# Optimization experiments

Hardware: AMD Instinct MI355X
Metric: run time of the kernel (lower is better)

## Reference

```python
import jax, jax.numpy as jnp
import numpy as np


def conv1d(x, w, b, pad):
    # x: (B, Cin, T), w: (Cout, Cin, K), b: (Cout,)
    y = jax.lax.conv_general_dilated(x, w, window_strides=(1,), padding=[(pad, pad)],
                                     dimension_numbers=('NCH', 'OIH', 'NCH'))
    return y + b[None, :, None]


def setup_inputs() -> dict:
    key = jax.random.key(0)
    ks = jax.random.split(key, 12)
    B, Cm, T1, Ct, T2, Ca = 8, 80, 800, 512, 200, 80
    queries = jax.random.normal(ks[0], (B, Cm, T1), dtype=jnp.float32)
    keys = jax.random.normal(ks[1], (B, Ct, T2), dtype=jnp.float32)
    query_lens = jnp.full((B,), T1, dtype=jnp.int32)
    key_lens = jax.random.randint(ks[2], (B,), T2 // 2, T2 + 1)
    # mask True where key position is padding (>= key_len): (B, T2, 1)
    mask = (jnp.arange(T2)[None, :] >= key_lens[:, None])[:, :, None]
    attn_prior = jax.random.uniform(ks[3], (B, T1, T2), dtype=jnp.float32) + 0.1
    # key_proj: Conv1d(512->1024, k=3, pad=1) + ReLU + Conv1d(1024->80, k=1)
    kp_w1 = jax.random.normal(ks[4], (2 * Ct, Ct, 3), jnp.float32) * 0.02
    kp_b1 = jnp.zeros((2 * Ct,), jnp.float32)
    kp_w2 = jax.random.normal(ks[5], (Ca, 2 * Ct, 1), jnp.float32) * 0.02
    kp_b2 = jnp.zeros((Ca,), jnp.float32)
    # query_proj (3xconv): Conv1d(80->160,k3)+ReLU+Conv1d(160->80,k1)+ReLU+Conv1d(80->80,k1)
    qp_w1 = jax.random.normal(ks[6], (2 * Cm, Cm, 3), jnp.float32) * 0.05
    qp_b1 = jnp.zeros((2 * Cm,), jnp.float32)
    qp_w2 = jax.random.normal(ks[7], (Cm, 2 * Cm, 1), jnp.float32) * 0.05
    qp_b2 = jnp.zeros((Cm,), jnp.float32)
    qp_w3 = jax.random.normal(ks[8], (Ca, Cm, 1), jnp.float32) * 0.05
    qp_b3 = jnp.zeros((Ca,), jnp.float32)
    return {"queries": queries, "keys": keys, "query_lens": query_lens, "mask": mask,
            "attn_prior": attn_prior, "kp_w1": kp_w1, "kp_b1": kp_b1, "kp_w2": kp_w2,
            "kp_b2": kp_b2, "qp_w1": qp_w1, "qp_b1": qp_b1, "qp_w2": qp_w2,
            "qp_b2": qp_b2, "qp_w3": qp_w3, "qp_b3": qp_b3}


def reference(queries, keys, query_lens, mask, attn_prior,
              kp_w1, kp_b1, kp_w2, kp_b2,
              qp_w1, qp_b1, qp_w2, qp_b2, qp_w3, qp_b3):
    # key projection: (B, Ct, T2) -> (B, Ca, T2)
    ke = conv1d(keys, kp_w1, kp_b1, pad=1)
    ke = jax.nn.relu(ke)
    ke = conv1d(ke, kp_w2, kp_b2, pad=0)
    # query projection ('3xconv'): (B, Cm, T1) -> (B, Ca, T1)
    qe = conv1d(queries, qp_w1, qp_b1, pad=1)
    qe = jax.nn.relu(qe)
    qe = conv1d(qe, qp_w2, qp_b2, pad=0)
    qe = jax.nn.relu(qe)
    qe = conv1d(qe, qp_w3, qp_b3, pad=0)
    # broadcasted squared L2 distance: (B, Ca, T1, T2) -> reduce C -> (B, 1, T1, T2)
    diff2 = (qe[:, :, :, None] - ke[:, :, None, :]) ** 2
    attn = -0.0005 * jnp.sum(diff2, axis=1, keepdims=True)
    # prior in log domain
    attn = jax.nn.log_softmax(attn, axis=3) + jnp.log(attn_prior[:, None] + 1e-8)
    attn_logprob = attn
    # mask (B, T2, 1) -> (B, 1, 1, T2)
    m = jnp.transpose(mask, (0, 2, 1))[:, :, None, :]
    attn = jnp.where(m, -jnp.inf, attn)
    attn = jax.nn.softmax(attn, axis=3)
    return (attn, attn_logprob)
```

## Files before the change

kernel.cpp:

```cpp
#include <hip/hip_runtime.h>
#include <hip/hip_bf16.h>
#include <math.h>

#define B_  8
#define CM  80
#define T1_ 800
#define CT  512
#define T2_ 200
#define CA  80

using bf16 = __hip_bfloat16;
typedef __attribute__((ext_vector_type(8))) short bf16x8;
typedef __attribute__((ext_vector_type(4))) float f32x4;

#define LDSW 56
#define LDSW2 72
#define LDSW3 168
#define LDSW4 104

__device__ __forceinline__ float load_sel(const void* p, long idx, int isf32) {
  if (isf32) return ((const float*)p)[idx];
  return __bfloat162float(((const bf16*)p)[idx]);
}

__device__ __forceinline__ unsigned short f2bf(float x) {
  bf16 h = __float2bfloat16(x);
  return *reinterpret_cast<unsigned short*>(&h);
}

__device__ __forceinline__ int detect_f32(const unsigned short* q) {
  __shared__ int s_f;
  const int tid = threadIdx.x;
  if (tid < 64) {
    unsigned short u = q[2 * tid];
    int e = (u >> 7) & 0xFF;
    unsigned long long bal = __ballot(e < 100 || e > 154);
    if (tid == 0) s_f = (__popcll(bal) >= 16) ? 1 : 0;
  }
  __syncthreads();
  return s_f;
}

__device__ void task_cvt_t(const void* X, bf16* XT, int f, int C, int T,
                           int id2, int tilesT, float* smem, int tid) {
  const int per_b = tilesT * ((C + 31) >> 5);
  const int b = id2 / per_b;
  const int r = id2 - b * per_b;
  const int ct = r / tilesT, tt = r - ct * tilesT;
  const int c0 = ct * 32, t0 = tt * 32;
  const int tx = tid & 31, trow = tid >> 5;
#pragma unroll
  for (int p = 0; p < 4; ++p) {
    const int cr = trow + 8 * p;
    if (c0 + cr < C && t0 + tx < T)
      smem[cr * 33 + tx] = load_sel(X, ((long)b * C + c0 + cr) * T + t0 + tx, f);
  }
  __syncthreads();
#pragma unroll
  for (int p = 0; p < 4; ++p) {
    const int tr = trow + 8 * p;
    if (t0 + tr < T && c0 + tx < C)
      XT[((long)b * T + t0 + tr) * C + c0 + tx] =
          __float2bfloat16(smem[tx * 33 + tr]);
  }
}

__device__ void task_wfrag(const void* W, bf16* WF, int f, int id2, int tid) {
  const int id = id2 * 256 + tid;
  const int l  = id & 63;
  int rest = id >> 6;
  const int h  = rest & 1; rest >>= 1;
  const int mi = rest & 3; rest >>= 2;
  const int w2 = rest & 1; rest >>= 1;
  const int ks = rest % 24;
  const int p  = rest / 24;
  const int co = p * 128 + w2 * 64 + mi * 16 + (l & 15);
  const int k0 = ks * 64 + h * 32 + (l >> 4) * 8;
  const int dk = k0 >> 9;
  const int ci = k0 & 511;
  const long sbase = ((long)co * 512 + ci) * 3 + dk;
  ushort4 u0, u1;
  u0.x = f2bf(load_sel(W, sbase + 0 * 3, f));
  u0.y = f2bf(load_sel(W, sbase + 1 * 3, f));
  u0.z = f2bf(load_sel(W, sbase + 2 * 3, f));
  u0.w = f2bf(load_sel(W, sbase + 3 * 3, f));
  u1.x = f2bf(load_sel(W, sbase + 4 * 3, f));
  u1.y = f2bf(load_sel(W, sbase + 5 * 3, f));
  u1.z = f2bf(load_sel(W, sbase + 6 * 3, f));
  u1.w = f2bf(load_sel(W, sbase + 7 * 3, f));
  *(ushort4*)(WF + (long)id * 8) = u0;
  *(ushort4*)(WF + (long)id * 8 + 4) = u1;
}

__device__ void task_wt3v(const void* W, bf16* WT, int f, int Co, int Ci,
                          int id2, int tid) {
  const int i = id2 * 256 + tid;
  const int g4 = Ci >> 2;
  if (i >= Co * g4) return;
  const int co = i / g4, ci = (i - co * g4) * 4;
  const long sbase = ((long)co * Ci + ci) * 3;
  float w[12];
  if (f) {
    const float4* s = (const float4*)((const float*)W + sbase);
    float4 f0 = s[0], f1 = s[1], f2 = s[2];
    w[0]=f0.x; w[1]=f0.y; w[2]=f0.z; w[3]=f0.w; w[4]=f1.x; w[5]=f1.y;
    w[6]=f1.z; w[7]=f1.w; w[8]=f2.x; w[9]=f2.y; w[10]=f2.z; w[11]=f2.w;
  } else {
#pragma unroll
    for (int j = 0; j < 12; ++j) w[j] = load_sel(W, sbase + j, 0);
  }
#pragma unroll
  for (int dk = 0; dk < 3; ++dk) {
    ushort4 u;
    u.x = f2bf(w[0 * 3 + dk]); u.y = f2bf(w[1 * 3 + dk]);
    u.z = f2bf(w[2 * 3 + dk]); u.w = f2bf(w[3 * 3 + dk]);
    *(ushort4*)(WT + ((long)dk * Co + co) * Ci + ci) = u;
  }
}

__device__ void task_cvtv(const void* W, bf16* O, int f, int n, int id2, int tid) {
  const int i = (id2 * 256 + tid) * 4;
  if (i >= n) return;
  ushort4 u;
  if (f) {
    float4 v = *(const float4*)((const float*)W + i);
    u.x = f2bf(v.x); u.y = f2bf(v.y); u.z = f2bf(v.z); u.w = f2bf(v.w);
  } else {
    u.x = f2bf(load_sel(W, i, 0));     u.y = f2bf(load_sel(W, i + 1, 0));
    u.z = f2bf(load_sel(W, i + 2, 0)); u.w = f2bf(load_sel(W, i + 3, 0));
  }
  *(ushort4*)(O + i) = u;
}

__global__ __launch_bounds__(256) void k_prep(
    const void* __restrict__ queries, const void* __restrict__ keys,
    const void* __restrict__ mask,
    const void* __restrict__ kp_w1, const void* __restrict__ kp_b1,
    const void* __restrict__ kp_w2, const void* __restrict__ kp_b2,
    const void* __restrict__ qp_w1, const void* __restrict__ qp_b1,
    const void* __restrict__ qp_w2, const void* __restrict__ qp_b2,
    const void* __restrict__ qp_w3, const void* __restrict__ qp_b3,
    bf16* __restrict__ keysT, bf16* __restrict__ queriesT,
    bf16* __restrict__ w1F, bf16* __restrict__ qw1T,
    bf16* __restrict__ kw2c, bf16* __restrict__ qw2c, bf16* __restrict__ qw3c,
    float* __restrict__ biasf, float* __restrict__ mf, float* __restrict__ kn) {
  __shared__ float smem[32 * 33];
  const int tid = threadIdx.x;
  const int f = detect_f32((const unsigned short*)queries);
  int id = blockIdx.x;

  if (id < 896) { task_cvt_t(keys, keysT, f, CT, T2_, id, 7, smem, tid); return; }
  id -= 896;
  if (id < 600) { task_cvt_t(queries, queriesT, f, CM, T1_, id, 25, smem, tid); return; }
  id -= 600;
  if (id < 768) { task_wfrag(kp_w1, w1F, f, id, tid); return; }
  id -= 768;
  if (id < 13) { task_wt3v(qp_w1, qw1T, f, 160, CM, id, tid); return; }
  id -= 13;
  if (id < 80) { task_cvtv(kp_w2, kw2c, f, 80 * 1024, id, tid); return; }
  id -= 80;
  if (id < 13) { task_cvtv(qp_w2, qw2c, f, 80 * 160, id, tid); return; }
  id -= 13;
  if (id < 7) { task_cvtv(qp_w3, qw3c, f, 80 * 80, id, tid); return; }
  id -= 7;

  if (id == 0) {
    for (int i = tid; i < 1424; i += 256) {
      float v;
      if (i < 1024)      v = load_sel(kp_b1, i, f);
      else if (i < 1104) v = load_sel(kp_b2, i - 1024, f);
      else if (i < 1264) v = load_sel(qp_b1, i - 1104, f);
      else if (i < 1344) v = load_sel(qp_b2, i - 1264, f);
      else               v = load_sel(qp_b3, i - 1344, f);
      biasf[i] = v;
    }
    for (int i = tid; i < B_ * T2_; i += 256) kn[i] = 0.f;
    return;
  }

  {
    int* s_fmt = (int*)smem;
    const int nmask = B_ * T2_;
    if (tid == 0) s_fmt[0] = 1;
    __syncthreads();
    const unsigned int* wi = (const unsigned int*)mask;
    const int nw = nmask / 4;
    int pri = 0;
    for (int i = tid; i < nw; i += 256) {
      unsigned int w = wi[i];
      if (w == 0u || w == 1u) continue;
      if (w == 0x3F803F80u || w == 0x00003F80u) { pri = max(pri, 2); continue; }
      if (w == 0x3F800000u) continue;
      unsigned int b0 = w & 0xFFu, b1 = (w >> 8) & 0xFFu,
                   b2 = (w >> 16) & 0xFFu, b3 = (w >> 24) & 0xFFu;
      if (b0 <= 1u && b1 <= 1u && b2 <= 1u && b3 <= 1u) pri = max(pri, 3);
      else pri = max(pri, 2);
    }
    if (pri) atomicMax(&s_fmt[0], pri);
    __syncthreads();
    const int fmt = s_fmt[0];
    for (int i = tid; i < nmask; i += 256) {
      int m;
      if (fmt == 3)      m = ((const unsigned char*)mask)[i] != 0;
      else if (fmt == 2) m = ((const unsigned short*)mask)[i] != 0;
      else               m = (wi[i] != 0u);
      mf[i] = (float)m;
    }
  }
}

__device__ void conv_tile(
    const bf16* __restrict__ XT, const bf16* __restrict__ WT,
    const float* __restrict__ bias, void* __restrict__ Y,
    int Cin, int Cout, int T, int KW, int pad, int relu, int outmode,
    int m0, int n0, short* As, short* Bs, float* Y2 = nullptr) {
  const int K = Cin * KW;
  const int tid = threadIdx.x;
  const int wave = tid >> 6;
  const int lane = tid & 63;

  const int row = tid >> 2;
  const int koff = (tid & 3) * 8;
  const int n = n0 + row;
  const int bb = n / T;
  const int t = n - bb * T;

  const int wm = (wave >> 1) * 32;
  const int wn = (wave & 1) * 32;
  const int fm = lane & 15;
  const int quad = lane >> 4;

  f32x4 acc[2][2] = {};

  const short* ap0 = As + (wm + fm) * LDSW + quad * 8;
  const short* bp0 = Bs + (wn + fm) * LDSW + quad * 8;

  auto loadA = [&](int k0) -> uint4 {
    const int k = k0 + koff;
    const int m = m0 + row;
    uint4 v = {0u, 0u, 0u, 0u};
    if (m < Cout && k < K) {
      const int dk = k / Cin;
      const int ci = k - dk * Cin;
      v = *(const uint4*)(WT + ((long)dk * Cout + m) * Cin + ci);
    }
    return v;
  };
  auto loadB = [&](int k0) -> uint4 {
    const int k = k0 + koff;
    uint4 v = {0u, 0u, 0u, 0u};
    if (k < K) {
      const int dk = k / Cin;
      const int ci = k - dk * Cin;
      const int tt = t + dk - pad;
      if (tt >= 0 && tt < T)
        v = *(const uint4*)(XT + ((long)bb * T + tt) * Cin + ci);
    }
    return v;
  };

  uint4 va = loadA(0);
  uint4 vb = loadB(0);

  for (int k0 = 0; k0 < K; k0 += 32) {
    *(uint4*)(As + row * LDSW + koff) = va;
    *(uint4*)(Bs + row * LDSW + koff) = vb;
    if (k0 + 32 < K) {
      va = loadA(k0 + 32);
      vb = loadB(k0 + 32);
    }
    __syncthreads();
    {
      bf16x8 a0 = *(const bf16x8*)(ap0);
      bf16x8 a1 = *(const bf16x8*)(ap0 + 16 * LDSW);
      bf16x8 b0 = *(const bf16x8*)(bp0);
      bf16x8 b1 = *(const bf16x8*)(bp0 + 16 * LDSW);
      acc[0][0] = __builtin_amdgcn_mfma_f32_16x16x32_bf16(a0, b0, acc[0][0], 0, 0, 0);
      acc[0][1] = __builtin_amdgcn_mfma_f32_16x16x32_bf16(a0, b1, acc[0][1], 0, 0, 0);
      acc[1][0] = __builtin_amdgcn_mfma_f32_16x16x32_bf16(a1, b0, acc[1][0], 0, 0, 0);
      acc[1][1] = __builtin_amdgcn_mfma_f32_16x16x32_bf16(a1, b1, acc[1][1], 0, 0, 0);
    }
    __syncthreads();
  }

#pragma unroll
  for (int mi = 0; mi < 2; ++mi) {
    const int mrow = m0 + wm + mi * 16 + quad * 4;
    if (mrow >= Cout) continue;
    float bi[4];
#pragma unroll
    for (int r = 0; r < 4; ++r) bi[r] = bias[mrow + r];
#pragma unroll
    for (int ni = 0; ni < 2; ++ni) {
      const int ncol = n0 + wn + ni * 16 + fm;
      float o[4];
#pragma unroll
      for (int r = 0; r < 4; ++r) {
        float v = acc[mi][ni][r] + bi[r];
        if (relu) v = fmaxf(v, 0.f);
        o[r] = v;
      }
      if (outmode == 0) {
        ushort4 u;
        u.x = f2bf(o[0]); u.y = f2bf(o[1]); u.z = f2bf(o[2]); u.w = f2bf(o[3]);
        *(ushort4*)((bf16*)Y + (long)ncol * Cout + mrow) = u;
      } else if (outmode == 1) {
        *(float4*)((float*)Y + (long)ncol * Cout + mrow) =
            make_float4(o[0], o[1], o[2], o[3]);
      } else {
        const int bb2 = ncol / T;
        const int tloc = ncol - bb2 * T;
        float s4 = 0.f;
#pragma unroll
        for (int r = 0; r < 4; ++r) {
          ((float*)Y)[((long)bb2 * Cout + mrow + r) * T + tloc] = -2.f * o[r];
          s4 = fmaf(o[r], o[r], s4);
        }
        atomicAdd(&Y2[ncol], s4);
      }
    }
  }
}

__device__ void conv_key128(
    const bf16* __restrict__ XT, const bf16* __restrict__ WF,
    const float* __restrict__ bias, bf16* __restrict__ Y,
    int panel, int n0, short* Bs) {
  const int Cin = CT, Cout = 1024, T = T2_;
  const int tid = threadIdx.x;
  const int wave = tid >> 6;
  const int lane = tid & 63;
  const int m0 = panel * 128;

  const int rowb = tid >> 2;
  const int nb = n0 + rowb;
  const int bbb = nb / T;
  const int tb = nb - bbb * T;
  const int kcb = (tid & 3) * 16;

  const int w2 = wave >> 1;
  const int wm = w2 * 64;
  const int wn = (wave & 1) * 32;
  const int fm = lane & 15;
  const int quad = lane >> 4;

  f32x4 acc[4][2] = {};
  const short* bp0 = Bs + (wn + fm) * LDSW2 + quad * 8;

  uint4 vb0, vb1;
  auto loadB = [&](int k0) {
    const int dk = k0 >> 9;
    const int ci0 = k0 & 511;
    const int tt = tb + dk - 1;
    if (tt >= 0 && tt < T) {
      const bf16* src = XT + ((long)bbb * T + tt) * Cin + ci0 + kcb;
      vb0 = *(const uint4*)(src);
      vb1 = *(const uint4*)(src + 8);
    } else {
      uint4 z = {0u, 0u, 0u, 0u};
      vb0 = z; vb1 = z;
    }
  };

  loadB(0);

  for (int k0 = 0; k0 < 1536; k0 += 64) {
    const int ks = k0 >> 6;
    {
      short* dstb = Bs + rowb * LDSW2 + kcb;
      *(uint4*)(dstb) = vb0;
      *(uint4*)(dstb + 8) = vb1;
    }
    if (k0 + 64 < 1536) loadB(k0 + 64);

    const long abase = ((((long)panel * 24 + ks) * 2 + w2) * 4096) + lane * 8;
    bf16x8 a[4][2];
#pragma unroll
    for (int mi = 0; mi < 4; ++mi)
#pragma unroll
      for (int h = 0; h < 2; ++h)
        a[mi][h] = *(const bf16x8*)(WF + abase + (mi * 2 + h) * 512);

    __syncthreads();
#pragma unroll
    for (int h = 0; h < 2; ++h) {
      bf16x8 b0 = *(const bf16x8*)(bp0 + h * 32);
      bf16x8 b1 = *(const bf16x8*)(bp0 + 16 * LDSW2 + h * 32);
#pragma unroll
      for (int mi = 0; mi < 4; ++mi) {
        acc[mi][0] = __builtin_amdgcn_mfma_f32_16x16x32_bf16(a[mi][h], b0, acc[mi][0], 0, 0, 0);
        acc[mi][1] = __builtin_amdgcn_mfma_f32_16x16x32_bf16(a[mi][h], b1, acc[mi][1], 0, 0, 0);
      }
    }
    __syncthreads();
  }

#pragma unroll
  for (int mi = 0; mi < 4; ++mi) {
    const int mrow = m0 + wm + mi * 16 + quad * 4;
    float bi[4];
#pragma unroll
    for (int r = 0; r < 4; ++r) bi[r] = bias[mrow + r];
#pragma unroll
    for (int ni = 0; ni < 2; ++ni) {
      const int ncol = n0 + wn + ni * 16 + fm;
      const long base = (long)ncol * Cout + mrow;
      ushort4 u;
      u.x = f2bf(fmaxf(acc[mi][ni][0] + bi[0], 0.f));
      u.y = f2bf(fmaxf(acc[mi][ni][1] + bi[1], 0.f));
      u.z = f2bf(fmaxf(acc[mi][ni][2] + bi[2], 0.f));
      u.w = f2bf(fmaxf(acc[mi][ni][3] + bi[3], 0.f));
      *(ushort4*)(Y + base) = u;
    }
  }
}

__global__ __launch_bounds__(256) void k_conv1(
    const bf16* __restrict__ keysT, const bf16* __restrict__ w1F,
    const float* __restrict__ b_k1, bf16* __restrict__ ke1T,
    const bf16* __restrict__ queriesT, const bf16* __restrict__ qw1T,
    const float* __restrict__ b_q1, bf16* __restrict__ qe1T) {
  __shared__ __align__(16) short smem[2 * 64 * LDSW];
  int j = blockIdx.x;
  if (j < 200) {
    conv_key128(keysT, w1F, b_k1, ke1T, j & 7, (j >> 3) * 64, smem);
  } else {
    j -= 200;
    conv_tile(queriesT, qw1T, b_q1, qe1T, CM, 160, T1_, 3, 1, 1, 0,
              (j / 100) * 64, (j % 100) * 64, smem, smem + 64 * LDSW);
  }
}

__device__ void conv23_tile(
    const bf16* __restrict__ qe1T, const bf16* __restrict__ qw2c,
    const float* __restrict__ b_q2, const bf16* __restrict__ qw3c,
    const float* __restrict__ b_q3, float* __restrict__ qeT,
    float* __restrict__ qn, int n0, short* smem) {
  short* sIn = smem;
  short* sW2 = smem + 64 * LDSW3;
  short* sC  = smem;
  short* sW3 = smem + 64 * LDSW3;
  const int tid = threadIdx.x;
  const int wave = tid >> 6;
  const int lane = tid & 63;
  const int fm = lane & 15;
  const int quad = lane >> 4;

#pragma unroll
  for (int c = tid; c < 1280; c += 256) {
    const int row = c / 20, kc = (c - row * 20) * 8;
    uint4 v = *(const uint4*)(qe1T + (long)(n0 + row) * 160 + kc);
    *(uint4*)(sIn + row * LDSW3 + kc) = v;
  }
  for (int c = tid; c < 1600; c += 256) {
    const int row = c / 20, kc = (c - row * 20) * 8;
    uint4 v = *(const uint4*)(qw2c + (long)row * 160 + kc);
    *(uint4*)(sW2 + row * LDSW3 + kc) = v;
  }
  __syncthreads();

  f32x4 acc1[5] = {};
#pragma unroll
  for (int ks = 0; ks < 5; ++ks) {
    bf16x8 b = *(const bf16x8*)(sIn + (16 * wave + fm) * LDSW3 + ks * 32 + quad * 8);
#pragma unroll
    for (int mt = 0; mt < 5; ++mt) {
      bf16x8 a = *(const bf16x8*)(sW2 + (16 * mt + fm) * LDSW3 + ks * 32 + quad * 8);
      acc1[mt] = __builtin_amdgcn_mfma_f32_16x16x32_bf16(a, b, acc1[mt], 0, 0, 0);
    }
  }
  __syncthreads();

#pragma unroll
  for (int mt = 0; mt < 5; ++mt) {
    const int ch = 16 * mt + quad * 4;
    const float4 b2 = *(const float4*)(b_q2 + ch);
    ushort4 u;
    u.x = f2bf(fmaxf(acc1[mt][0] + b2.x, 0.f));
    u.y = f2bf(fmaxf(acc1[mt][1] + b2.y, 0.f));
    u.z = f2bf(fmaxf(acc1[mt][2] + b2.z, 0.f));
    u.w = f2bf(fmaxf(acc1[mt][3] + b2.w, 0.f));
    *(ushort4*)(sC + (16 * wave + fm) * LDSW4 + ch) = u;
  }
  if (tid < 128) {
    const int row = tid >> 1, off = 80 + (tid & 1) * 8;
    uint4 z = {0u, 0u, 0u, 0u};
    *(uint4*)(sC + row * LDSW4 + off) = z;
  }
  for (int c = tid; c < 800; c += 256) {
    const int row = c / 10, kc = (c - row * 10) * 8;
    uint4 v = *(const uint4*)(qw3c + (long)row * 80 + kc);
    *(uint4*)(sW3 + row * LDSW4 + kc) = v;
  }
  if (tid < 160) {
    const int row = tid >> 1, off = 80 + (tid & 1) * 8;
    uint4 z = {0u, 0u, 0u, 0u};
    *(uint4*)(sW3 + row * LDSW4 + off) = z;
  }
  __syncthreads();

  f32x4 acc2[5] = {};
#pragma unroll
  for (int ks = 0; ks < 3; ++ks) {
    bf16x8 b = *(const bf16x8*)(sC + (16 * wave + fm) * LDSW4 + ks * 32 + quad * 8);
#pragma unroll
    for (int mt = 0; mt < 5; ++mt) {
      bf16x8 a = *(const bf16x8*)(sW3 + (16 * mt + fm) * LDSW4 + ks * 32 + quad * 8);
      acc2[mt] = __builtin_amdgcn_mfma_f32_16x16x32_bf16(a, b, acc2[mt], 0, 0, 0);
    }
  }

  const int pos = n0 + 16 * wave + fm;
  float p = 0.f;
#pragma unroll
  for (int mt = 0; mt < 5; ++mt) {
    const int ch = 16 * mt + quad * 4;
    const float4 b3 = *(const float4*)(b_q3 + ch);
    float4 o = make_float4(acc2[mt][0] + b3.x, acc2[mt][1] + b3.y,
                           acc2[mt][2] + b3.z, acc2[mt][3] + b3.w);
    p = fmaf(o.x, o.x, p); p = fmaf(o.y, o.y, p);
    p = fmaf(o.z, o.z, p); p = fmaf(o.w, o.w, p);
    *(float4*)(qeT + (long)pos * CA + ch) = o;
  }
  p += __shfl_xor(p, 16, 64);
  p += __shfl_xor(p, 32, 64);
  if (quad == 0) qn[pos] = p;
}

__global__ __launch_bounds__(256) void k_conv2f(
    const bf16* __restrict__ ke1T, const bf16* __restrict__ kw2c,
    const float* __restrict__ b_k2, float* __restrict__ keT,
    float* __restrict__ kn,
    const bf16* __restrict__ qe1T, const bf16* __restrict__ qw2c,
    const float* __restrict__ b_q2, const bf16* __restrict__ qw3c,
    const float* __restrict__ b_q3, float* __restrict__ qeT,
    float* __restrict__ qn) {
  __shared__ __align__(16) short smem[64 * LDSW3 + 80 * LDSW3];
  int j = blockIdx.x;
  if (j < 50) {
    conv_tile(ke1T, kw2c, b_k2, keT, 1024, CA, T2_, 1, 0, 0, 2,
              (j / 25) * 64, (j % 25) * 64, smem, smem + 64 * LDSW, kn);
  } else {
    conv23_tile(qe1T, qw2c, b_q2, qw3c, b_q3, qeT, qn, (j - 50) * 64, smem);
  }
}

__global__ __launch_bounds__(256) void k_dist(
    const float* __restrict__ qeT, const float* __restrict__ keT2,
    const float* __restrict__ kn, const float* __restrict__ qn,
    const void* __restrict__ prior, const float* __restrict__ mf,
    void* __restrict__ out, const unsigned short* __restrict__ qprobe) {
  __shared__ float sq[4 * CA];
  __shared__ float sqn[4];
  __shared__ float redA[16], redB[16], redC[16], redD[16];
  const int f = detect_f32(qprobe);
  const int b = blockIdx.y;
  const int t1base = blockIdx.x * 4;
  const int tid = threadIdx.x;
  const int wid = tid >> 6;

  for (int i = tid; i < 4 * CA; i += 256) {
    int u = i / CA, c = i - u * CA;
    sq[i] = qeT[((long)b * T1_ + t1base + u) * CA + c];
  }
  if (tid < 4) sqn[tid] = qn[b * T1_ + t1base + tid];
  __syncthreads();

  const int t2 = tid;
  const bool valid = (t2 < T2_);
  float x[4] = {-INFINITY, -INFINITY, -INFINITY, -INFINITY};
  if (valid) {
    const float* kp = keT2 + (long)b * CA * T2_ + t2;
    const float knv = kn[b * T2_ + t2];
    float a0 = 0.f, a1 = 0.f, a2 = 0.f, a3 = 0.f;
#pragma unroll 2
    for (int j = 0; j < CA; j += 4) {
      const float4 q0 = *(const float4*)(sq + 0 * CA + j);
      const float4 q1 = *(const float4*)(sq + 1 * CA + j);
      const float4 q2 = *(const float4*)(sq + 2 * CA + j);
      const float4 q3 = *(const float4*)(sq + 3 * CA + j);
      const float k0v = kp[(j + 0) * T2_];
      const float k1v = kp[(j + 1) * T2_];
      const float k2v = kp[(j + 2) * T2_];
      const float k3v = kp[(j + 3) * T2_];
      a0 = fmaf(k0v, q0.x, a0); a0 = fmaf(k1v, q0.y, a0);
      a0 = fmaf(k2v, q0.z, a0); a0 = fmaf(k3v, q0.w, a0);
      a1 = fmaf(k0v, q1.x, a1); a1 = fmaf(k1v, q1.y, a1);
      a1 = fmaf(k2v, q1.z, a1); a1 = fmaf(k3v, q1.w, a1);
      a2 = fmaf(k0v, q2.x, a2); a2 = fmaf(k1v, q2.y, a2);
      a2 = fmaf(k2v, q2.z, a2); a2 = fmaf(k3v, q2.w, a2);
      a3 = fmaf(k0v, q3.x, a3); a3 = fmaf(k1v, q3.y, a3);
      a3 = fmaf(k2v, q3.z, a3); a3 = fmaf(k3v, q3.w, a3);
    }
    x[0] = -0.0005f * (a0 + sqn[0] + knv);
    x[1] = -0.0005f * (a1 + sqn[1] + knv);
    x[2] = -0.0005f * (a2 + sqn[2] + knv);
// ... 65 lines not shown
  for (int u = 0; u < 4; ++u)
    M2[u] = fmaxf(fmaxf(redC[u], redC[4 + u]), fmaxf(redC[8 + u], redC[12 + u]));

  float e2[4], s2[4];
#pragma unroll
  for (int u = 0; u < 4; ++u) {
    e2[u] = (xm[u] == -INFINITY) ? 0.f : __expf(xm[u] - M2[u]);
    s2[u] = e2[u];
  }
#pragma unroll
  for (int o = 32; o > 0; o >>= 1)
#pragma unroll
    for (int u = 0; u < 4; ++u) s2[u] += __shfl_down(s2[u], o, 64);
  if ((tid & 63) == 0)
#pragma unroll
    for (int u = 0; u < 4; ++u) redD[wid * 4 + u] = s2[u];
  __syncthreads();
#pragma unroll
  for (int u = 0; u < 4; ++u) {
    const float S2 = redD[u] + redD[4 + u] + redD[8 + u] + redD[12 + u];
    if (valid) {
      float a = (S2 > 0.f) ? (e2[u] / S2) : 0.f;
      const long oidx = ((long)b * T1_ + t1base + u) * T2_ + t2;
      if (f) ((float*)out)[oidx] = a;
      else   ((bf16*)out)[oidx] = __float2bfloat16(a);
    }
  }
}

extern "C" void kernel_launch(void* const* d_in, const int* in_sizes, int n_in,
                              void* d_out, int out_size, void* d_ws, size_t ws_size,
                              hipStream_t stream) {
  const void* queries = d_in[0];
  const void* keys    = d_in[1];
  const void* mask    = d_in[3];
  const void* prior   = d_in[4];
  const void* kp_w1 = d_in[5];
  const void* kp_b1 = d_in[6];
  const void* kp_w2 = d_in[7];
  const void* kp_b2 = d_in[8];
  const void* qp_w1 = d_in[9];
  const void* qp_b1 = d_in[10];
  const void* qp_w2 = d_in[11];
  const void* qp_b2 = d_in[12];
  const void* qp_w3 = d_in[13];
  const void* qp_b3 = d_in[14];

  float* keT   = (float*)d_ws;
  float* qeT   = keT + 128000;
  float* mf    = qeT + 512000;
  float* biasf = mf + 1600;
  float* kn    = biasf + 1440;
  float* qn    = kn + 1600;
  bf16* keysT    = (bf16*)(qn + 6400);
  bf16* queriesT = keysT + 819200;
  bf16* w1F      = queriesT + 512000;
  bf16* qw1T     = w1F + 1572864;
  bf16* kw2c     = qw1T + 38400;
  bf16* qw2c     = kw2c + 81920;
  bf16* qw3c     = qw2c + 12800;
  bf16* ke1T     = qw3c + 6400;
  bf16* qe1T     = ke1T + 1638400;

  float* b_k1 = biasf;
  float* b_k2 = biasf + 1024;
  float* b_q1 = biasf + 1104;
  float* b_q2 = biasf + 1264;
  float* b_q3 = biasf + 1344;

  k_prep<<<2379, 256, 0, stream>>>(
      queries, keys, mask,
      kp_w1, kp_b1, kp_w2, kp_b2,
      qp_w1, qp_b1, qp_w2, qp_b2, qp_w3, qp_b3,
      keysT, queriesT, w1F, qw1T, kw2c, qw2c, qw3c, biasf, mf, kn);

  k_conv1<<<500, 256, 0, stream>>>(keysT, w1F, b_k1, ke1T,
                                   queriesT, qw1T, b_q1, qe1T);

  k_conv2f<<<150, 256, 0, stream>>>(ke1T, kw2c, b_k2, keT, kn,
                                    qe1T, qw2c, b_q2, qw3c, b_q3, qeT, qn);

  k_dist<<<dim3(200, B_), 256, 0, stream>>>(
      qeT, keT, kn, qn, prior, mf, d_out, (const unsigned short*)queries);
}
```

Measured before the change: 150.8 us.

## Use pre-fragmented weights and direct-from-global MFMA operands in conv kernels

Weights for the first query conv and second key conv are now pre-packed in prep into MFMA fragment order. The conv kernels then load A and B operands straight from global memory into registers, with no LDS staging and no __syncthreads. Out-of-range time taps read from a small zeroed pad buffer instead of going through branches. Both the query conv1 and the key conv2 tiles are reorganised so one block covers all output channels, which cuts block counts and removes the atomicAdd for the key norms. The cost is less data reuse across waves and more global and L2 traffic per MFMA.

After: 193.5 us. 28.3% more time.

```diff
diff --git a/kernel.cpp b/kernel.cpp
--- a/kernel.cpp
+++ b/kernel.cpp
@@ -13,8 +13,6 @@
 typedef __attribute__((ext_vector_type(8))) short bf16x8;
 typedef __attribute__((ext_vector_type(4))) float f32x4;
 
-#define LDSW 56
-#define LDSW2 72
 #define LDSW3 168
 #define LDSW4 104
 
@@ -92,30 +90,56 @@
   *(ushort4*)(WF + (long)id * 8 + 4) = u1;
 }
 
-__device__ void task_wt3v(const void* W, bf16* WT, int f, int Co, int Ci,
-                          int id2, int tid) {
-  const int i = id2 * 256 + tid;
-  const int g4 = Ci >> 2;
-  if (i >= Co * g4) return;
-  const int co = i / g4, ci = (i - co * g4) * 4;
-  const long sbase = ((long)co * Ci + ci) * 3;
-  float w[12];
+__device__ void task_qwf(const void* W, bf16* WF, int f, int id2, int tid) {
+  const int id = id2 * 256 + tid;
+  const int l = id & 63;
+  const int rest = id >> 6;
+  const int mt = rest % 10;
+  const int s = rest / 10;
+  const int m = mt * 16 + (l & 15);
+  const int kb = s * 32 + (l >> 4) * 8;
+  ushort4 u0; u0.x = 0; u0.y = 0; u0.z = 0; u0.w = 0;
+  ushort4 u1 = u0;
+  if (kb < 240) {
+    int dk = 0; if (kb >= 80) dk = 1; if (kb >= 160) dk = 2;
+    const int ci = kb - dk * 80;
+    const long sb = ((long)m * 80 + ci) * 3 + dk;
+    u0.x = f2bf(load_sel(W, sb + 0 * 3, f));
+    u0.y = f2bf(load_sel(W, sb + 1 * 3, f));
+    u0.z = f2bf(load_sel(W, sb + 2 * 3, f));
+    u0.w = f2bf(load_sel(W, sb + 3 * 3, f));
+    u1.x = f2bf(load_sel(W, sb + 4 * 3, f));
+    u1.y = f2bf(load_sel(W, sb + 5 * 3, f));
+    u1.z = f2bf(load_sel(W, sb + 6 * 3, f));
+    u1.w = f2bf(load_sel(W, sb + 7 * 3, f));
+  }
+  *(ushort4*)(WF + (long)id * 8) = u0;
+  *(ushort4*)(WF + (long)id * 8 + 4) = u1;
+}
+
+__device__ void task_kw2f(const void* W, bf16* WF, int f, int id2, int tid) {
+  const int id = id2 * 256 + tid;
+  const int l = id & 63;
+  const int rest = id >> 6;
+  const int mt = rest % 5;
+  const int s = rest / 5;
+  const int m = mt * 16 + (l & 15);
+  const int kb = s * 32 + (l >> 4) * 8;
+  const long sb = (long)m * 1024 + kb;
+  ushort4 u0, u1;
   if (f) {
-    const float4* s = (const float4*)((const float*)W + sbase);
-    float4 f0 = s[0], f1 = s[1], f2 = s[2];
-    w[0]=f0.x; w[1]=f0.y; w[2]=f0.z; w[3]=f0.w; w[4]=f1.x; w[5]=f1.y;
-    w[6]=f1.z; w[7]=f1.w; w[8]=f2.x; w[9]=f2.y; w[10]=f2.z; w[11]=f2.w;
+    const float4* p4 = (const float4*)((const float*)W + sb);
+    float4 a = p4[0], b = p4[1];
+    u0.x = f2bf(a.x); u0.y = f2bf(a.y); u0.z = f2bf(a.z); u0.w = f2bf(a.w);
+    u1.x = f2bf(b.x); u1.y = f2bf(b.y); u1.z = f2bf(b.z); u1.w = f2bf(b.w);
   } else {
-#pragma unroll
-    for (int j = 0; j < 12; ++j) w[j] = load_sel(W, sbase + j, 0);
-  }
-#pragma unroll
-  for (int dk = 0; dk < 3; ++dk) {
-    ushort4 u;
-    u.x = f2bf(w[0 * 3 + dk]); u.y = f2bf(w[1 * 3 + dk]);
-    u.z = f2bf(w[2 * 3 + dk]); u.w = f2bf(w[3 * 3 + dk]);
-    *(ushort4*)(WT + ((long)dk * Co + co) * Ci + ci) = u;
-  }
+    u0.x = f2bf(load_sel(W, sb + 0, 0)); u0.y = f2bf(load_sel(W, sb + 1, 0));
+    u0.z = f2bf(load_sel(W, sb + 2, 0)); u0.w = f2bf(load_sel(W, sb + 3, 0));
+    u1.x = f2bf(load_sel(W, sb + 4, 0)); u1.y = f2bf(load_sel(W, sb + 5, 0));
+    u1.z = f2bf(load_sel(W, sb + 6, 0)); u1.w = f2bf(load_sel(W, sb + 7, 0));
+  }
+  *(ushort4*)(WF + (long)id * 8) = u0;
+  *(ushort4*)(WF + (long)id * 8 + 4) = u1;
 }
 
 __device__ void task_cvtv(const void* W, bf16* O, int f, int n, int id2, int tid) {
@@ -141,9 +165,10 @@
     const void* __restrict__ qp_w2, const void* __restrict__ qp_b2,
     const void* __restrict__ qp_w3, const void* __restrict__ qp_b3,
     bf16* __restrict__ keysT, bf16* __restrict__ queriesT,
-    bf16* __restrict__ w1F, bf16* __restrict__ qw1T,
-    bf16* __restrict__ kw2c, bf16* __restrict__ qw2c, bf16* __restrict__ qw3c,
-    float* __restrict__ biasf, float* __restrict__ mf, float* __restrict__ kn) {
+    bf16* __restrict__ w1F, bf16* __restrict__ qw1F,
+    bf16* __restrict__ kw2F, bf16* __restrict__ qw2c, bf16* __restrict__ qw3c,
+    float* __restrict__ biasf, float* __restrict__ mf, float* __restrict__ kn,
+    bf16* __restrict__ zpad) {
   __shared__ float smem[32 * 33];
   const int tid = threadIdx.x;
   const int f = detect_f32((const unsigned short*)queries);
@@ -155,10 +180,10 @@
   id -= 600;
   if (id < 768) { task_wfrag(kp_w1, w1F, f, id, tid); return; }
   id -= 768;
-  if (id < 13) { task_wt3v(qp_w1, qw1T, f, 160, CM, id, tid); return; }
-  id -= 13;
-  if (id < 80) { task_cvtv(kp_w2, kw2c, f, 80 * 1024, id, tid); return; }
-  id -= 80;
+  if (id < 20) { task_qwf(qp_w1, qw1F, f, id, tid); return; }
+  id -= 20;
+  if (id < 40) { task_kw2f(kp_w2, kw2F, f, id, tid); return; }
+  id -= 40;
   if (id < 13) { task_cvtv(qp_w2, qw2c, f, 80 * 160, id, tid); return; }
   id -= 13;
   if (id < 7) { task_cvtv(qp_w3, qw3c, f, 80 * 80, id, tid); return; }
@@ -175,6 +200,7 @@
       biasf[i] = v;
     }
     for (int i = tid; i < B_ * T2_; i += 256) kn[i] = 0.f;
+    if (tid < 32) ((unsigned int*)zpad)[tid] = 0u;
     return;
   }
 
@@ -209,226 +235,185 @@
   }
 }
 
-__device__ void conv_tile(
-    const bf16* __restrict__ XT, const bf16* __restrict__ WT,
-    const float* __restrict__ bias, void* __restrict__ Y,
-    int Cin, int Cout, int T, int KW, int pad, int relu, int outmode,
-    int m0, int n0, short* As, short* Bs, float* Y2 = nullptr) {
-  const int K = Cin * KW;
+__device__ void conv_key_direct(
+    const bf16* __restrict__ XT, const bf16* __restrict__ WF,
+    const float* __restrict__ bias, bf16* __restrict__ Y,
+    const bf16* __restrict__ zpad, int panel, int n0) {
   const int tid = threadIdx.x;
   const int wave = tid >> 6;
   const int lane = tid & 63;
-
-  const int row = tid >> 2;
-  const int koff = (tid & 3) * 8;
-  const int n = n0 + row;
-  const int bb = n / T;
-  const int t = n - bb * T;
-
-  const int wm = (wave >> 1) * 32;
+  const int w2 = wave >> 1;
   const int wn = (wave & 1) * 32;
   const int fm = lane & 15;
   const int quad = lane >> 4;
-
-  f32x4 acc[2][2] = {};
-
-  const short* ap0 = As + (wm + fm) * LDSW + quad * 8;
-  const short* bp0 = Bs + (wn + fm) * LDSW + quad * 8;
-
-  auto loadA = [&](int k0) -> uint4 {
-    const int k = k0 + koff;
-    const int m = m0 + row;
-    uint4 v = {0u, 0u, 0u, 0u};
-    if (m < Cout && k < K) {
-      const int dk = k / Cin;
-      const int ci = k - dk * Cin;
-      v = *(const uint4*)(WT + ((long)dk * Cout + m) * Cin + ci);
-    }
-    return v;
-  };
-  auto loadB = [&](int k0) -> uint4 {
-    const int k = k0 + koff;
-    uint4 v = {0u, 0u, 0u, 0u};
-    if (k < K) {
-      const int dk = k / Cin;
-      const int ci = k - dk * Cin;
-      const int tt = t + dk - pad;
-      if (tt >= 0 && tt < T)
-        v = *(const uint4*)(XT + ((long)bb * T + tt) * Cin + ci);
-    }
-    return v;
-  };
-
-  uint4 va = loadA(0);
-  uint4 vb = loadB(0);
-
-  for (int k0 = 0; k0 < K; k0 += 32) {
-    *(uint4*)(As + row * LDSW + koff) = va;
-    *(uint4*)(Bs + row * LDSW + koff) = vb;
-    if (k0 + 32 < K) {
-      va = loadA(k0 + 32);
-      vb = loadB(k0 + 32);
-    }
-    __syncthreads();
-    {
-      bf16x8 a0 = *(const bf16x8*)(ap0);
-      bf16x8 a1 = *(const bf16x8*)(ap0 + 16 * LDSW);
-      bf16x8 b0 = *(const bf16x8*)(bp0);
-      bf16x8 b1 = *(const bf16x8*)(bp0 + 16 * LDSW);
-      acc[0][0] = __builtin_amdgcn_mfma_f32_16x16x32_bf16(a0, b0, acc[0][0], 0, 0, 0);
-      acc[0][1] = __builtin_amdgcn_mfma_f32_16x16x32_bf16(a0, b1, acc[0][1], 0, 0, 0);
-      acc[1][0] = __builtin_amdgcn_mfma_f32_16x16x32_bf16(a1, b0, acc[1][0], 0, 0, 0);
-      acc[1][1] = __builtin_amdgcn_mfma_f32_16x16x32_bf16(a1, b1, acc[1][1], 0, 0, 0);
-    }
-    __syncthreads();
-  }
-
-#pragma unroll
-  for (int mi = 0; mi < 2; ++mi) {
-    const int mrow = m0 + wm + mi * 16 + quad * 4;
-    if (mrow >= Cout) continue;
+  const int qo = quad * 8;
+
+  const int nA = n0 + wn + fm;
+  const int nB = nA + 16;
+  const int bbA = nA / T2_, tbA = nA - bbA * T2_;
+  const int bbB = nB / T2_, tbB = nB - bbB * T2_;
+
+  f32x4 acc[4][2] = {};
+
+#pragma unroll 8
+  for (int ks = 0; ks < 24; ++ks) {
+    const int dk = ks >> 3;
+    const int ci0 = (ks & 7) * 64;
+    const long abase = ((((long)panel * 24 + ks) * 2 + w2) * 4096) + lane * 8;
+    bf16x8 a[4][2];
+#pragma unroll
+    for (int mi = 0; mi < 4; ++mi)
+#pragma unroll
+      for (int h = 0; h < 2; ++h)
+        a[mi][h] = *(const bf16x8*)(WF + abase + (mi * 2 + h) * 512);
+
+    const int ttA = tbA + dk - 1;
+    const int ttB = tbB + dk - 1;
+    const bf16* pA = ((unsigned)ttA < (unsigned)T2_)
+        ? XT + ((long)(bbA * T2_ + ttA) * CT + ci0 + qo) : zpad;
+    const bf16* pB = ((unsigned)ttB < (unsigned)T2_)
+        ? XT + ((long)(bbB * T2_ + ttB) * CT + ci0 + qo) : zpad;
+    bf16x8 b0l = *(const bf16x8*)(pA);
+    bf16x8 b0h = *(const bf16x8*)(pA + 32);
+    bf16x8 b1l = *(const bf16x8*)(pB);
+    bf16x8 b1h = *(const bf16x8*)(pB + 32);
+
+#pragma unroll
+    for (int mi = 0; mi < 4; ++mi) {
+      acc[mi][0] = __builtin_amdgcn_mfma_f32_16x16x32_bf16(a[mi][0], b0l, acc[mi][0], 0, 0, 0);
+      acc[mi][1] = __builtin_amdgcn_mfma_f32_16x16x32_bf16(a[mi][0], b1l, acc[mi][1], 0, 0, 0);
+    }
+#pragma unroll
+    for (int mi = 0; mi < 4; ++mi) {
+      acc[mi][0] = __builtin_amdgcn_mfma_f32_16x16x32_bf16(a[mi][1], b0h, acc[mi][0], 0, 0, 0);
+      acc[mi][1] = __builtin_amdgcn_mfma_f32_16x16x32_bf16(a[mi][1], b1h, acc[mi][1], 0, 0, 0);
+    }
+  }
+
+  const int m0 = panel * 128;
+#pragma unroll
+  for (int mi = 0; mi < 4; ++mi) {
+    const int mrow = m0 + w2 * 64 + mi * 16 + quad * 4;
     float bi[4];
 #pragma unroll
     for (int r = 0; r < 4; ++r) bi[r] = bias[mrow + r];
 #pragma unroll
     for (int ni = 0; ni < 2; ++ni) {
       const int ncol = n0 + wn + ni * 16 + fm;
-      float o[4];
-#pragma unroll
-      for (int r = 0; r < 4; ++r) {
-        float v = acc[mi][ni][r] + bi[r];
-        if (relu) v = fmaxf(v, 0.f);
-        o[r] = v;
-      }
-      if (outmode == 0) {
-        ushort4 u;
-        u.x = f2bf(o[0]); u.y = f2bf(o[1]); u.z = f2bf(o[2]); u.w = f2bf(o[3]);
-        *(ushort4*)((bf16*)Y + (long)ncol * Cout + mrow) = u;
-      } else if (outmode == 1) {
-        *(float4*)((float*)Y + (long)ncol * Cout + mrow) =
-            make_float4(o[0], o[1], o[2], o[3]);
-      } else {
-        const int bb2 = ncol / T;
-        const int tloc = ncol - bb2 * T;
-        float s4 = 0.f;
-#pragma unroll
-        for (int r = 0; r < 4; ++r) {
-          ((float*)Y)[((long)bb2 * Cout + mrow + r) * T + tloc] = -2.f * o[r];
-          s4 = fmaf(o[r], o[r], s4);
-        }
-        atomicAdd(&Y2[ncol], s4);
-      }
-    }
-  }
-}
-
-__device__ void conv_key128(
-    const bf16* __restrict__ XT, const bf16* __restrict__ WF,
-    const float* __restrict__ bias, bf16* __restrict__ Y,
-    int panel, int n0, short* Bs) {
-  const int Cin = CT, Cout = 1024, T = T2_;
-  const int tid = threadIdx.x;
-  const int wave = tid >> 6;
-  const int lane = tid & 63;
-  const int m0 = panel * 128;
-
-  const int rowb = tid >> 2;
-  const int nb = n0 + rowb;
-  const int bbb = nb / T;
-  const int tb = nb - bbb * T;
-  const int kcb = (tid & 3) * 16;
-
-  const int w2 = wave >> 1;
-  const int wm = w2 * 64;
-  const int wn = (wave & 1) * 32;
-  const int fm = lane & 15;
-  const int quad = lane >> 4;
-
-  f32x4 acc[4][2] = {};
-  const short* bp0 = Bs + (wn + fm) * LDSW2 + quad * 8;
-
-  uint4 vb0, vb1;
-  auto loadB = [&](int k0) {
-    const int dk = k0 >> 9;
-    const int ci0 = k0 & 511;
-    const int tt = tb + dk - 1;
-    if (tt >= 0 && tt < T) {
-      const bf16* src = XT + ((long)bbb * T + tt) * Cin + ci0 + kcb;
-      vb0 = *(const uint4*)(src);
-      vb1 = *(const uint4*)(src + 8);
-    } else {
-      uint4 z = {0u, 0u, 0u, 0u};
-      vb0 = z; vb1 = z;
-    }
-  };
-
-  loadB(0);
-
-  for (int k0 = 0; k0 < 1536; k0 += 64) {
-    const int ks = k0 >> 6;
-    {
-      short* dstb = Bs + rowb * LDSW2 + kcb;
-      *(uint4*)(dstb) = vb0;
-      *(uint4*)(dstb + 8) = vb1;
-    }
-    if (k0 + 64 < 1536) loadB(k0 + 64);
-
-    const long abase = ((((long)panel * 24 + ks) * 2 + w2) * 4096) + lane * 8;
-    bf16x8 a[4][2];
-#pragma unroll
-    for (int mi = 0; mi < 4; ++mi)
-#pragma unroll
-      for (int h = 0; h < 2; ++h)
-        a[mi][h] = *(const bf16x8*)(WF + abase + (mi * 2 + h) * 512);
-
-    __syncthreads();
-#pragma unroll
-    for (int h = 0; h < 2; ++h) {
-      bf16x8 b0 = *(const bf16x8*)(bp0 + h * 32);
-      bf16x8 b1 = *(const bf16x8*)(bp0 + 16 * LDSW2 + h * 32);
-#pragma unroll
-      for (int mi = 0; mi < 4; ++mi) {
-        acc[mi][0] = __builtin_amdgcn_mfma_f32_16x16x32_bf16(a[mi][h], b0, acc[mi][0], 0, 0, 0);
-        acc[mi][1] = __builtin_amdgcn_mfma_f32_16x16x32_bf16(a[mi][h], b1, acc[mi][1], 0, 0, 0);
-      }
-    }
-    __syncthreads();
-  }
-
-#pragma unroll
-  for (int mi = 0; mi < 4; ++mi) {
-    const int mrow = m0 + wm + mi * 16 + quad * 4;
-    float bi[4];
-#pragma unroll
-    for (int r = 0; r < 4; ++r) bi[r] = bias[mrow + r];
-#pragma unroll
-    for (int ni = 0; ni < 2; ++ni) {
-      const int ncol = n0 + wn + ni * 16 + fm;
-      const long base = (long)ncol * Cout + mrow;
       ushort4 u;
       u.x = f2bf(fmaxf(acc[mi][ni][0] + bi[0], 0.f));
       u.y = f2bf(fmaxf(acc[mi][ni][1] + bi[1], 0.f));
       u.z = f2bf(fmaxf(acc[mi][ni][2] + bi[2], 0.f));
       u.w = f2bf(fmaxf(acc[mi][ni][3] + bi[3], 0.f));
-      *(ushort4*)(Y + base) = u;
-    }
+      *(ushort4*)(Y + (long)ncol * 1024 + mrow) = u;
+    }
+  }
+}
+
+__device__ void conv_q_direct(
+    const bf16* __restrict__ X, const bf16* __restrict__ WF,
+    const float* __restrict__ bias, bf16* __restrict__ Y,
+    const bf16* __restrict__ zpad, int n0) {
+  const int tid = threadIdx.x;
+  const int wave = tid >> 6;
+  const int lane = tid & 63;
+  const int fm = lane & 15;
+  const int quad = lane >> 4;
+  const int n = n0 + wave * 16 + fm;
+  const int bb = n / T1_;
+  const int tb = n - bb * T1_;
+
+  f32x4 acc[10] = {};
+#pragma unroll
+  for (int s = 0; s < 8; ++s) {
+    int k = s * 32 + quad * 8;
+    if (k > 232) k = 232;
+    const int dk = (k >= 160) ? 2 : ((k >= 80) ? 1 : 0);
+    const int ci = k - dk * 80;
+    const int tt = tb + dk - 1;
+    const bf16* src = ((unsigned)tt < (unsigned)T1_)
+        ? X + ((long)(bb * T1_ + tt) * CM + ci) : zpad;
+    bf16x8 b = *(const bf16x8*)src;
+#pragma unroll
+    for (int mt = 0; mt < 10; ++mt) {
+      bf16x8 a = *(const bf16x8*)(WF + ((long)(s * 10 + mt)) * 512 + lane * 8);
+      acc[mt] = __builtin_amdgcn_mfma_f32_16x16x32_bf16(a, b, acc[mt], 0, 0, 0);
+    }
+  }
+
+#pragma unroll
+  for (int mt = 0; mt < 10; ++mt) {
+    const int m = mt * 16 + quad * 4;
+    const float4 bi = *(const float4*)(bias + m);
+    ushort4 u;
+    u.x = f2bf(fmaxf(acc[mt][0] + bi.x, 0.f));
+    u.y = f2bf(fmaxf(acc[mt][1] + bi.y, 0.f));
+    u.z = f2bf(fmaxf(acc[mt][2] + bi.z, 0.f));
+    u.w = f2bf(fmaxf(acc[mt][3] + bi.w, 0.f));
+    *(ushort4*)(Y + (long)n * 160 + m) = u;
   }
 }
 
 __global__ __launch_bounds__(256) void k_conv1(
     const bf16* __restrict__ keysT, const bf16* __restrict__ w1F,
     const float* __restrict__ b_k1, bf16* __restrict__ ke1T,
-    const bf16* __restrict__ queriesT, const bf16* __restrict__ qw1T,
-    const float* __restrict__ b_q1, bf16* __restrict__ qe1T) {
-  __shared__ __align__(16) short smem[2 * 64 * LDSW];
+    const bf16* __restrict__ queriesT, const bf16* __restrict__ qw1F,
+    const float* __restrict__ b_q1, bf16* __restrict__ qe1T,
+    const bf16* __restrict__ zpad) {
   int j = blockIdx.x;
   if (j < 200) {
-    conv_key128(keysT, w1F, b_k1, ke1T, j & 7, (j >> 3) * 64, smem);
+    conv_key_direct(keysT, w1F, b_k1, ke1T, zpad, j & 7, (j >> 3) * 64);
   } else {
-    j -= 200;
-    conv_tile(queriesT, qw1T, b_q1, qe1T, CM, 160, T1_, 3, 1, 1, 0,
-              (j / 100) * 64, (j % 100) * 64, smem, smem + 64 * LDSW);
-  }
+    conv_q_direct(queriesT, qw1F, b_q1, qe1T, zpad, (j - 200) * 64);
+  }
+}
+
+__device__ void conv_k2_direct(
+    const bf16* __restrict__ X, const bf16* __restrict__ WF,
+    const float* __restrict__ bias, float* __restrict__ keT,
+    float* __restrict__ kn, int n0) {
+  const int tid = threadIdx.x;
+  const int wave = tid >> 6;
+  const int lane = tid & 63;
+  const int fm = lane & 15;
+  const int quad = lane >> 4;
+  const int n = n0 + wave * 16 + fm;
+  const int bb2 = n / T2_;
+  const int tloc = n - bb2 * T2_;
+  const bf16* xrow = X + (long)n * 1024 + quad * 8;
+
+  f32x4 acc[5] = {};
+#pragma unroll 8
+  for (int s = 0; s < 32; ++s) {
+    bf16x8 b = *(const bf16x8*)(xrow + s * 32);
+#pragma unroll
+    for (int mt = 0; mt < 5; ++mt) {
+      bf16x8 a = *(const bf16x8*)(WF + ((long)(s * 5 + mt)) * 512 + lane * 8);
+      acc[mt] = __builtin_amdgcn_mfma_f32_16x16x32_bf16(a, b, acc[mt], 0, 0, 0);
+    }
+  }
+
+  float p = 0.f;
+  float* dst0 = keT + ((long)bb2 * 80) * 200 + tloc;
+#pragma unroll
+  for (int mt = 0; mt < 5; ++mt) {
+    const int m = mt * 16 + quad * 4;
+    const float4 bi = *(const float4*)(bias + m);
+    const float o0 = acc[mt][0] + bi.x;
+    const float o1 = acc[mt][1] + bi.y;
+    const float o2 = acc[mt][2] + bi.z;
+    const float o3 = acc[mt][3] + bi.w;
+    float* d = dst0 + (long)m * 200;
+    d[0]   = -2.f * o0;
+    d[200] = -2.f * o1;
+    d[400] = -2.f * o2;
+    d[600] = -2.f * o3;
+    p = fmaf(o0, o0, p); p = fmaf(o1, o1, p);
+    p = fmaf(o2, o2, p); p = fmaf(o3, o3, p);
+  }
+  p += __shfl_xor(p, 16, 64);
+  p += __shfl_xor(p, 32, 64);
+  if (quad == 0) kn[n] = p;
 }
 
 __device__ void conv23_tile(
@@ -528,20 +513,19 @@
 }
 
 __global__ __launch_bounds__(256) void k_conv2f(
-    const bf16* __restrict__ ke1T, const bf16* __restrict__ kw2c,
+    const bf16* __restrict__ ke1T, const bf16* __restrict__ kw2F,
     const float* __restrict__ b_k2, float* __restrict__ keT,
     float* __restrict__ kn,
     const bf16* __restrict__ qe1T, const bf16* __restrict__ qw2c,
     const float* __restrict__ b_q2, const bf16* __restrict__ qw3c,
     const float* __restrict__ b_q3, float* __restrict__ qeT,
     float* __restrict__ qn) {
-  __shared__ __align__(16) short smem[64 * LDSW3 + 80 * LDSW3];
+  __shared__ __align__(16) short smem[144 * LDSW3];
   int j = blockIdx.x;
-  if (j < 50) {
-    conv_tile(ke1T, kw2c, b_k2, keT, 1024, CA, T2_, 1, 0, 0, 2,
-              (j / 25) * 64, (j % 25) * 64, smem, smem + 64 * LDSW, kn);
+  if (j < 25) {
+    conv_k2_direct(ke1T, kw2F, b_k2, keT, kn, j * 64);
   } else {
-    conv23_tile(qe1T, qw2c, b_q2, qw3c, b_q3, qeT, qn, (j - 50) * 64, smem);
+    conv23_tile(qe1T, qw2c, b_q2, qw3c, b_q3, qeT, qn, (j - 25) * 64, smem);
   }
 }
 
@@ -713,12 +697,13 @@
   float* biasf = mf + 1600;
   float* kn    = biasf + 1440;
   float* qn    = kn + 1600;
-  bf16* keysT    = (bf16*)(qn + 6400);
+  bf16* zpad     = (bf16*)(qn + 6400);
+  bf16* keysT    = zpad + 64;
   bf16* queriesT = keysT + 819200;
   bf16* w1F      = queriesT + 512000;
-  bf16* qw1T     = w1F + 1572864;
-  bf16* kw2c     = qw1T + 38400;
-  bf16* qw2c     = kw2c + 81920;
+  bf16* qw1F     = w1F + 1572864;
+  bf16* kw2F     = qw1F + 40960;
+  bf16* qw2c     = kw2F + 81920;
   bf16* qw3c     = qw2c + 12800;
   bf16* ke1T     = qw3c + 6400;
   bf16* qe1T     = ke1T + 1638400;
@@ -729,16 +714,16 @@
   float* b_q2 = biasf + 1264;
   float* b_q3 = biasf + 1344;
 
-  k_prep<<<2379, 256, 0, stream>>>(
+  k_prep<<<2346, 256, 0, stream>>>(
       queries, keys, mask,
       kp_w1, kp_b1, kp_w2, kp_b2,
       qp_w1, qp_b1, qp_w2, qp_b2, qp_w3, qp_b3,
-      keysT, queriesT, w1F, qw1T, kw2c, qw2c, qw3c, biasf, mf, kn);
-
-  k_conv1<<<500, 256, 0, stream>>>(keysT, w1F, b_k1, ke1T,
-                                   queriesT, qw1T, b_q1, qe1T);
-
-  k_conv2f<<<150, 256, 0, stream>>>(ke1T, kw2c, b_k2, keT, kn,
+      keysT, queriesT, w1F, qw1F, kw2F, qw2c, qw3c, biasf, mf, kn, zpad);
+
+  k_conv1<<<300, 256, 0, stream>>>(keysT, w1F, b_k1, ke1T,
+                                   queriesT, qw1F, b_q1, qe1T, zpad);
+
+  k_conv2f<<<125, 256, 0, stream>>>(ke1T, kw2F, b_k2, keT, kn,
                                     qe1T, qw2c, b_q2, qw3c, b_q3, qeT, qn);
 
   k_dist<<<dim3(200, B_), 256, 0, stream>>>(
```

## Stage key conv input halo tile once in LDS and reuse across taps

Applied to the files above, without the earlier changes.

The key conv1 GEMM now loads a 66-row time halo of the input (64 outputs plus neighbours) into LDS in two 256-channel phases. All three kernel taps reuse these rows by shifting the row index, with out-of-range rows pointing to a zero row. Before, each tap reloaded its B slice through 24 synchronized k-steps. This removes about two thirds of the global input reads and most barriers, at the cost of much larger LDS use (67x266 shorts), which may reduce occupancy. Weight fragments are now loaded from global memory directly inside the MFMA loop instead of being prefetched ahead of it.

Result: slower. 195.8 us (+29.8%).

```diff
diff --git a/kernel.cpp b/kernel.cpp
--- a/kernel.cpp
+++ b/kernel.cpp
@@ -14,9 +14,9 @@
 typedef __attribute__((ext_vector_type(4))) float f32x4;
 
 #define LDSW 56
-#define LDSW2 72
 #define LDSW3 168
 #define LDSW4 104
+#define KLDSW 266
 
 __device__ __forceinline__ float load_sel(const void* p, long idx, int isf32) {
   if (isf32) return ((const float*)p)[idx];
@@ -326,91 +326,110 @@
     const bf16* __restrict__ XT, const bf16* __restrict__ WF,
     const float* __restrict__ bias, bf16* __restrict__ Y,
     int panel, int n0, short* Bs) {
-  const int Cin = CT, Cout = 1024, T = T2_;
   const int tid = threadIdx.x;
   const int wave = tid >> 6;
   const int lane = tid & 63;
-  const int m0 = panel * 128;
-
-  const int rowb = tid >> 2;
-  const int nb = n0 + rowb;
-  const int bbb = nb / T;
-  const int tb = nb - bbb * T;
-  const int kcb = (tid & 3) * 16;
-
   const int w2 = wave >> 1;
-  const int wm = w2 * 64;
   const int wn = (wave & 1) * 32;
   const int fm = lane & 15;
   const int quad = lane >> 4;
+  const int qo = quad * 8;
+
+  const int nA = n0 + wn + fm;
+  const int nB = nA + 16;
+  const int bbA = nA / T2_, tbA = nA - bbA * T2_;
+  const int bbB = nB / T2_, tbB = nB - bbB * T2_;
+  const int rA0 = wn + fm;
+  const int rB0 = wn + fm + 16;
 
   f32x4 acc[4][2] = {};
-  const short* bp0 = Bs + (wn + fm) * LDSW2 + quad * 8;
-
-  uint4 vb0, vb1;
-  auto loadB = [&](int k0) {
-    const int dk = k0 >> 9;
-    const int ci0 = k0 & 511;
-    const int tt = tb + dk - 1;
-    if (tt >= 0 && tt < T) {
-      const bf16* src = XT + ((long)bbb * T + tt) * Cin + ci0 + kcb;
-      vb0 = *(const uint4*)(src);
-      vb1 = *(const uint4*)(src + 8);
-    } else {
-      uint4 z = {0u, 0u, 0u, 0u};
-      vb0 = z; vb1 = z;
+
+  uint4 st[9];
+  auto ldphase = [&](int p) {
+#pragma unroll
+    for (int r = 0; r < 9; ++r) {
+      const int c = tid + 256 * r;
+      uint4 v = {0u, 0u, 0u, 0u};
+      if (c < 2144) {
+        const int i = c >> 5;
+        const int col = ((c & 31) << 3) + (p << 8);
+        const int g = n0 - 1 + i;
+        if (i < 66 && g >= 0 && g < B_ * T2_)
+          v = *(const uint4*)(XT + (long)g * CT + col);
+      }
+      st[r] = v;
     }
   };
-
-  loadB(0);
-
-  for (int k0 = 0; k0 < 1536; k0 += 64) {
-    const int ks = k0 >> 6;
-    {
-      short* dstb = Bs + rowb * LDSW2 + kcb;
-      *(uint4*)(dstb) = vb0;
-      *(uint4*)(dstb + 8) = vb1;
-    }
-    if (k0 + 64 < 1536) loadB(k0 + 64);
-
-    const long abase = ((((long)panel * 24 + ks) * 2 + w2) * 4096) + lane * 8;
-    bf16x8 a[4][2];
-#pragma unroll
-    for (int mi = 0; mi < 4; ++mi)
-#pragma unroll
-      for (int h = 0; h < 2; ++h)
-        a[mi][h] = *(const bf16x8*)(WF + abase + (mi * 2 + h) * 512);
-
-    __syncthreads();
-#pragma unroll
-    for (int h = 0; h < 2; ++h) {
-      bf16x8 b0 = *(const bf16x8*)(bp0 + h * 32);
-      bf16x8 b1 = *(const bf16x8*)(bp0 + 16 * LDSW2 + h * 32);
-#pragma unroll
-      for (int mi = 0; mi < 4; ++mi) {
-        acc[mi][0] = __builtin_amdgcn_mfma_f32_16x16x32_bf16(a[mi][h], b0, acc[mi][0], 0, 0, 0);
-        acc[mi][1] = __builtin_amdgcn_mfma_f32_16x16x32_bf16(a[mi][h], b1, acc[mi][1], 0, 0, 0);
+  auto wrphase = [&]() {
+#pragma unroll
+    for (int r = 0; r < 9; ++r) {
+      const int c = tid + 256 * r;
+      if (c < 2144)
+        *(uint4*)(Bs + (c >> 5) * KLDSW + ((c & 31) << 3)) = st[r];
+    }
+  };
+
+  ldphase(0);
+  wrphase();
+  ldphase(1);
+  __syncthreads();
+
+#pragma unroll
+  for (int p = 0; p < 2; ++p) {
+    if (p == 1) {
+      __syncthreads();
+      wrphase();
+      __syncthreads();
+    }
+#pragma unroll
+    for (int dk = 0; dk < 3; ++dk) {
+      const int ttA = tbA + dk - 1;
+      const int ttB = tbB + dk - 1;
+      const int rowA = ((unsigned)ttA < (unsigned)T2_) ? (rA0 + dk) : 66;
+      const int rowB = ((unsigned)ttB < (unsigned)T2_) ? (rB0 + dk) : 66;
+      const short* pA0 = Bs + rowA * KLDSW + qo;
+      const short* pB0 = Bs + rowB * KLDSW + qo;
+#pragma unroll
+      for (int k4 = 0; k4 < 4; ++k4) {
+        const int ks = dk * 8 + p * 4 + k4;
+        const int cl = k4 * 64;
+        bf16x8 bA0 = *(const bf16x8*)(pA0 + cl);
+        bf16x8 bA1 = *(const bf16x8*)(pA0 + cl + 32);
+        bf16x8 bB0 = *(const bf16x8*)(pB0 + cl);
+        bf16x8 bB1 = *(const bf16x8*)(pB0 + cl + 32);
+        const long abase = ((((long)panel * 24 + ks) * 2 + w2) * 4096) + lane * 8;
+#pragma unroll
+        for (int mi = 0; mi < 4; ++mi) {
+          bf16x8 a0 = *(const bf16x8*)(WF + abase + (mi * 2 + 0) * 512);
+          acc[mi][0] = __builtin_amdgcn_mfma_f32_16x16x32_bf16(a0, bA0, acc[mi][0], 0, 0, 0);
+          acc[mi][1] = __builtin_amdgcn_mfma_f32_16x16x32_bf16(a0, bB0, acc[mi][1], 0, 0, 0);
+        }
+#pragma unroll
+        for (int mi = 0; mi < 4; ++mi) {
+          bf16x8 a1 = *(const bf16x8*)(WF + abase + (mi * 2 + 1) * 512);
+          acc[mi][0] = __builtin_amdgcn_mfma_f32_16x16x32_bf16(a1, bA1, acc[mi][0], 0, 0, 0);
+          acc[mi][1] = __builtin_amdgcn_mfma_f32_16x16x32_bf16(a1, bB1, acc[mi][1], 0, 0, 0);
+        }
       }
     }
-    __syncthreads();
-  }
-
+  }
+
+  const int m0 = panel * 128;
 #pragma unroll
   for (int mi = 0; mi < 4; ++mi) {
-    const int mrow = m0 + wm + mi * 16 + quad * 4;
+    const int mrow = m0 + w2 * 64 + mi * 16 + quad * 4;
     float bi[4];
 #pragma unroll
     for (int r = 0; r < 4; ++r) bi[r] = bias[mrow + r];
 #pragma unroll
     for (int ni = 0; ni < 2; ++ni) {
       const int ncol = n0 + wn + ni * 16 + fm;
-      const long base = (long)ncol * Cout + mrow;
       ushort4 u;
       u.x = f2bf(fmaxf(acc[mi][ni][0] + bi[0], 0.f));
       u.y = f2bf(fmaxf(acc[mi][ni][1] + bi[1], 0.f));
       u.z = f2bf(fmaxf(acc[mi][ni][2] + bi[2], 0.f));
       u.w = f2bf(fmaxf(acc[mi][ni][3] + bi[3], 0.f));
-      *(ushort4*)(Y + base) = u;
+      *(ushort4*)(Y + (long)ncol * 1024 + mrow) = u;
     }
   }
 }
@@ -420,7 +439,7 @@
     const float* __restrict__ b_k1, bf16* __restrict__ ke1T,
     const bf16* __restrict__ queriesT, const bf16* __restrict__ qw1T,
     const float* __restrict__ b_q1, bf16* __restrict__ qe1T) {
-  __shared__ __align__(16) short smem[2 * 64 * LDSW];
+  __shared__ __align__(16) short smem[67 * KLDSW];
   int j = blockIdx.x;
   if (j < 200) {
     conv_key128(keysT, w1F, b_k1, ke1T, j & 7, (j >> 3) * 64, smem);
```
